# Kernel tuning notes

Hardware: AMD Instinct MI355X
Metric: run time of the kernel (lower is better)

Reference implementation:

```python
import jax, jax.numpy as jnp
import numpy as np

VOCAB = 8192
ZC = 32
BETA = 0.25
EPS = 1e-12  # torch F.normalize eps


def l2norm(x):
    return x / jnp.maximum(jnp.linalg.norm(x, axis=-1, keepdims=True), EPS)


def setup_inputs() -> dict:
    key = jax.random.key(0)
    k1, k2 = jax.random.split(key)
    z = jax.random.normal(k1, (16, ZC, 32, 32), dtype=jnp.float32)  # [B, C, H, W]
    emb = jax.random.uniform(k2, (VOCAB, ZC), dtype=jnp.float32,
                             minval=-1.0 / VOCAB, maxval=1.0 / VOCAB)
    emb = l2norm(emb)  # codebook_norm init
    return {"z": z, "embedding": emb}


def reference(z, embedding):
    # b c h w -> b h w c
    zc = jnp.einsum('bchw->bhwc', z)
    z_flat = zc.reshape(-1, ZC)                      # [N, C], N = B*H*W
    # codebook_norm: normalize inputs and codebook
    z_flat = l2norm(z_flat)
    zn = z_flat.reshape(zc.shape)                    # normalized z, [B,H,W,C]
    e = l2norm(embedding)                            # [V, C]
    # squared euclidean distances: ||z||^2 + ||e||^2 - 2 z e^T  -> [N, V]
    d = (jnp.sum(z_flat ** 2, axis=1, keepdims=True)
         + jnp.sum(e ** 2, axis=1)
         - 2.0 * jnp.einsum('nd,vd->nv', z_flat, e))
    idx = jnp.argmin(d, axis=1)                      # [N]
    z_q = l2norm(embedding[idx]).reshape(zc.shape)   # gather + normalize
    commit_loss = BETA * jnp.mean((jax.lax.stop_gradient(z_q) - zn) ** 2)
    vq_loss = jnp.mean((z_q - jax.lax.stop_gradient(zn)) ** 2)
    # straight-through estimator
    z_q = zn + jax.lax.stop_gradient(z_q - zn)
    z_q = jnp.einsum('bhwc->bchw', z_q)
    return z_q, vq_loss, commit_loss
```

## Files before the change

kernel.cpp:

```cpp
#include <hip/hip_runtime.h>

typedef _Float16 f16;
typedef _Float16 f16x8 __attribute__((ext_vector_type(8)));
typedef float f32x4 __attribute__((ext_vector_type(4)));

#define ZC 32
#define HW 1024
#define TPB 256
#define VCH 256
#define ZROWS_BLK 256

__device__ __forceinline__ unsigned int fkey(float x) {
    unsigned int b = __float_as_uint(x);
    return (b & 0x80000000u) ? ~b : (b | 0x80000000u);
}

__global__ void kprep(const float* __restrict__ z, const float* __restrict__ emb,
                      float* __restrict__ e, f16* __restrict__ Eh, f16* __restrict__ El,
                      f16x8* __restrict__ ZFh, f16x8* __restrict__ ZFl,
                      unsigned long long* __restrict__ packed,
                      int N, int V, int zblocks) {
    const int blk = blockIdx.x;
    if (blk < zblocks) {
        int t = blk * TPB + threadIdx.x;
        if (t < N * 4) {
            int lane = t & 63, zt = t >> 6;
            int n = zt * 16 + (lane & 15);
            int b = n >> 10, hw = n & 1023;
            int kb = (lane >> 4) * 8;
            f16x8 h, l;
#pragma unroll
            for (int j = 0; j < 8; ++j) {
                float v = z[((size_t)(b * ZC + kb + j)) * HW + hw];
                f16 hh = (f16)v;
                h[j] = hh;
                l[j] = (f16)(v - (float)hh);
            }
            ZFh[t] = h;
            ZFl[t] = l;
        }
        int per = (N + zblocks - 1) / zblocks;
        int p0 = blk * per + threadIdx.x;
        if (threadIdx.x < per && p0 < N) packed[p0] = 0ull;
    } else {
        int r = (blk - zblocks) * TPB + threadIdx.x;
        if (r >= V) return;
        const float4* src = reinterpret_cast<const float4*>(emb) + (size_t)r * 8;
        float4 v[8];
        float s = 0.f;
#pragma unroll
        for (int j = 0; j < 8; ++j) {
            v[j] = src[j];
            s += v[j].x * v[j].x + v[j].y * v[j].y + v[j].z * v[j].z + v[j].w * v[j].w;
        }
        float inv = 1.0f / fmaxf(sqrtf(s), 1e-12f);
        float4* dst = reinterpret_cast<float4*>(e) + (size_t)r * 8;
        f16* eh = Eh + (size_t)r * ZC;
        f16* el = El + (size_t)r * ZC;
#pragma unroll
        for (int j = 0; j < 8; ++j) {
            float t0 = v[j].x * inv, t1 = v[j].y * inv, t2 = v[j].z * inv, t3 = v[j].w * inv;
            float4 o; o.x = t0; o.y = t1; o.z = t2; o.w = t3;
            dst[j] = o;
            f16 h0 = (f16)t0, h1 = (f16)t1, h2 = (f16)t2, h3 = (f16)t3;
            eh[4 * j + 0] = h0; eh[4 * j + 1] = h1; eh[4 * j + 2] = h2; eh[4 * j + 3] = h3;
            el[4 * j + 0] = (f16)(t0 - (float)h0);
            el[4 * j + 1] = (f16)(t1 - (float)h1);
            el[4 * j + 2] = (f16)(t2 - (float)h2);
            el[4 * j + 3] = (f16)(t3 - (float)h3);
        }
    }
}

__global__ __launch_bounds__(TPB, 4) void kmfma(const f16x8* __restrict__ ZFh,
                                                const f16x8* __restrict__ ZFl,
                                                const uint4* __restrict__ Eh,
                                                const uint4* __restrict__ El,
                                                unsigned long long* __restrict__ packed,
                                                int Vm1) {
    __shared__ uint4 sEh[VCH * 4];
    __shared__ uint4 sEl[VCH * 4];
    const int tid = threadIdx.x;
    const int zb = blockIdx.x & 63;
    const int cb = blockIdx.x >> 6;

    {
        const uint4* gh = Eh + (size_t)cb * (VCH * 4);
        const uint4* gl = El + (size_t)cb * (VCH * 4);
#pragma unroll
        for (int i = 0; i < 4; ++i) {
            int c = tid + i * TPB;
            int r = c >> 2, q = c & 3;
            int w = (r << 2) | (q ^ ((r >> 1) & 3));
            sEh[w] = gh[c];
            sEl[w] = gl[c];
        }
    }

    const int lane = tid & 63;
    const int wv = tid >> 6;
    const int zt0 = zb * 16 + wv * 4;

    f16x8 Bh[4], Bl[4];
#pragma unroll
    for (int i = 0; i < 4; ++i) {
        Bh[i] = ZFh[(size_t)(zt0 + i) * 64 + lane];
        Bl[i] = ZFl[(size_t)(zt0 + i) * 64 + lane];
    }
    __syncthreads();

    const int r15 = lane & 15, qq = lane >> 4;
    const int laneA = (r15 << 2) | (qq ^ ((r15 >> 1) & 3));

    float bv[4] = {-1e38f, -1e38f, -1e38f, -1e38f};
    int bi[4] = {0, 0, 0, 0};
    int g = cb * VCH + qq * 4;

    for (int ct = 0; ct < VCH / 16; ++ct) {
        f16x8 Ah = *(const f16x8*)&sEh[ct * 64 + laneA];
        f16x8 Al = *(const f16x8*)&sEl[ct * 64 + laneA];
#pragma unroll
        for (int i = 0; i < 4; ++i) {
            f32x4 acc = {0.f, 0.f, 0.f, 0.f};
            acc = __builtin_amdgcn_mfma_f32_16x16x32_f16(Ah, Bh[i], acc, 0, 0, 0);
            acc = __builtin_amdgcn_mfma_f32_16x16x32_f16(Ah, Bl[i], acc, 0, 0, 0);
            acc = __builtin_amdgcn_mfma_f32_16x16x32_f16(Al, Bh[i], acc, 0, 0, 0);
#pragma unroll
            for (int r = 0; r < 4; ++r) {
                float v = acc[r];
                bool gt = v > bv[i];
                bi[i] = gt ? (g + r) : bi[i];
                bv[i] = gt ? v : bv[i];
            }
        }
        g += 16;
    }

#pragma unroll
    for (int i = 0; i < 4; ++i) {
        unsigned long long key =
            ((unsigned long long)fkey(bv[i]) << 32) | (unsigned int)(Vm1 - bi[i]);
        unsigned long long o;
        o = __shfl_xor(key, 16); if (o > key) key = o;
        o = __shfl_xor(key, 32); if (o > key) key = o;
        if (lane < 16) atomicMax(&packed[(size_t)(zt0 + i) * 16 + r15], key);
    }
}

__global__ void kfinal(const float* __restrict__ z, const float* __restrict__ e,
                       const unsigned long long* __restrict__ packed,
                       float* __restrict__ out, float* __restrict__ partial, int V) {
    __shared__ float red[TPB];
    int n = blockIdx.x * TPB + threadIdx.x;
    int b = n >> 10, hw = n & 1023;
    unsigned long long p = packed[n];
    int idx = (V - 1) - (int)(unsigned int)(p & 0xFFFFFFFFull);

    float zrow[ZC];
    float s = 0.f;
#pragma unroll
    for (int c = 0; c < ZC; ++c) {
        float t = z[((size_t)b * ZC + c) * HW + hw];
        zrow[c] = t;
        s += t * t;
    }
    float inv = 1.0f / fmaxf(sqrtf(s), 1e-12f);

    const float4* er = reinterpret_cast<const float4*>(e) + (size_t)idx * 8;
    float loss = 0.f;
#pragma unroll
    for (int q = 0; q < 8; ++q) {
        float4 ev = er[q];
        float d0 = ev.x - zrow[4 * q + 0] * inv;
        float d1 = ev.y - zrow[4 * q + 1] * inv;
        float d2 = ev.z - zrow[4 * q + 2] * inv;
        float d3 = ev.w - zrow[4 * q + 3] * inv;
        loss += d0 * d0 + d1 * d1 + d2 * d2 + d3 * d3;
        out[((size_t)b * ZC + (4 * q + 0)) * HW + hw] = ev.x;
        out[((size_t)b * ZC + (4 * q + 1)) * HW + hw] = ev.y;
        out[((size_t)b * ZC + (4 * q + 2)) * HW + hw] = ev.z;
        out[((size_t)b * ZC + (4 * q + 3)) * HW + hw] = ev.w;
    }

    red[threadIdx.x] = loss;
    __syncthreads();
    for (int st = TPB / 2; st > 0; st >>= 1) {
        if (threadIdx.x < st) red[threadIdx.x] += red[threadIdx.x + st];
        __syncthreads();
    }
    if (threadIdx.x == 0) partial[blockIdx.x] = red[0];
}

__global__ void kloss(const float* __restrict__ partial, float* __restrict__ out,
                      int nblocks, int NC) {
    int lane = threadIdx.x;
    float s = (lane < nblocks) ? partial[lane] : 0.f;
#pragma unroll
    for (int off = 32; off > 0; off >>= 1) s += __shfl_down(s, off);
    if (lane == 0) {
        float mean = s / (float)NC;
        out[NC] = mean;
        out[NC + 1] = 0.25f * mean;
    }
}

extern "C" void kernel_launch(void* const* d_in, const int* in_sizes, int n_in,
                              void* d_out, int out_size, void* d_ws, size_t ws_size,
                              hipStream_t stream) {
    const float* z = (const float*)d_in[0];
    const float* emb = (const float*)d_in[1];
    float* out = (float*)d_out;

    const int N = in_sizes[0] / ZC;
    const int V = in_sizes[1] / ZC;

    char* ws = (char*)d_ws;
    float* e = (float*)ws;
    f16* Eh = (f16*)(ws + (size_t)V * ZC * 4);
    f16* El = (f16*)(ws + (size_t)V * ZC * 6);
    f16x8* ZFh = (f16x8*)(ws + (size_t)V * ZC * 8);
    f16x8* ZFl = (f16x8*)(ws + (size_t)V * ZC * 8 + (size_t)N * ZC * 2);
    unsigned long long* packed =
        (unsigned long long*)(ws + (size_t)V * ZC * 8 + (size_t)N * ZC * 4);
    float* partial = (float*)((char*)packed + (size_t)N * 8);

    const int zblocks = (N * 4 + TPB - 1) / TPB;
    const int eblocks = (V + TPB - 1) / TPB;

    kprep<<<zblocks + eblocks, TPB, 0, stream>>>(z, emb, e, Eh, El, ZFh, ZFl,
                                                 packed, N, V, zblocks);
    kmfma<<<(V / VCH) * (N / ZROWS_BLK), TPB, 0, stream>>>(
        ZFh, ZFl, (const uint4*)Eh, (const uint4*)El, packed, V - 1);
    kfinal<<<N / TPB, TPB, 0, stream>>>(z, e, packed, out, partial, V);
    kloss<<<1, 64, 0, stream>>>(partial, out, N / TPB, N * ZC);
}
```

Before: 42.29 us.

## Normalize z once in prep, double codebook chunk per block, reorder grid

The prep kernel now L2-normalizes each z row, using shuffles across the four lanes that share a row. It writes the normalized values as fp16 hi/lo MFMA operands and also as a row-major fp32 copy. The final kernel reads that copy instead of reloading strided z and recomputing the norm. The MFMA kernel doubles the codebook chunk per block to 512 entries, which halves the grid and doubles the shared memory per block; launch bounds drop to 2 blocks per CU and block indices put codebook chunks in the low bits. This cuts the number of atomicMax calls and the strided z traffic, at the cost of lower occupancy and an extra fp32 z buffer in memory.

Measured after the change: 46.03 us. +8.8%, slower.

```diff
diff --git a/kernel.cpp b/kernel.cpp
--- a/kernel.cpp
+++ b/kernel.cpp
@@ -7,7 +7,7 @@
 #define ZC 32
 #define HW 1024
 #define TPB 256
-#define VCH 256
+#define VCH 512
 #define ZROWS_BLK 256
 
 __device__ __forceinline__ unsigned int fkey(float x) {
@@ -18,30 +18,42 @@
 __global__ void kprep(const float* __restrict__ z, const float* __restrict__ emb,
                       float* __restrict__ e, f16* __restrict__ Eh, f16* __restrict__ El,
                       f16x8* __restrict__ ZFh, f16x8* __restrict__ ZFl,
+                      float* __restrict__ Zn,
                       unsigned long long* __restrict__ packed,
                       int N, int V, int zblocks) {
     const int blk = blockIdx.x;
     if (blk < zblocks) {
         int t = blk * TPB + threadIdx.x;
-        if (t < N * 4) {
-            int lane = t & 63, zt = t >> 6;
-            int n = zt * 16 + (lane & 15);
-            int b = n >> 10, hw = n & 1023;
-            int kb = (lane >> 4) * 8;
-            f16x8 h, l;
-#pragma unroll
-            for (int j = 0; j < 8; ++j) {
-                float v = z[((size_t)(b * ZC + kb + j)) * HW + hw];
-                f16 hh = (f16)v;
-                h[j] = hh;
-                l[j] = (f16)(v - (float)hh);
-            }
-            ZFh[t] = h;
-            ZFl[t] = l;
-        }
-        int per = (N + zblocks - 1) / zblocks;
-        int p0 = blk * per + threadIdx.x;
-        if (threadIdx.x < per && p0 < N) packed[p0] = 0ull;
+        int lane = t & 63, zt = t >> 6;
+        int n = zt * 16 + (lane & 15);
+        int b = n >> 10, hw = n & 1023;
+        int kb = (lane >> 4) * 8;
+        float x[8];
+        float s = 0.f;
+#pragma unroll
+        for (int j = 0; j < 8; ++j) {
+            x[j] = z[((size_t)(b * ZC + kb + j)) * HW + hw];
+            s += x[j] * x[j];
+        }
+        s += __shfl_xor(s, 16);
+        s += __shfl_xor(s, 32);
+        float inv = 1.0f / fmaxf(sqrtf(s), 1e-12f);
+        f16x8 h, l;
+        float4 zn0, zn1;
+#pragma unroll
+        for (int j = 0; j < 8; ++j) {
+            float xn = x[j] * inv;
+            f16 hh = (f16)xn;
+            h[j] = hh;
+            l[j] = (f16)(xn - (float)hh);
+            if (j < 4) ((float*)&zn0)[j] = xn; else ((float*)&zn1)[j - 4] = xn;
+        }
+        ZFh[t] = h;
+        ZFl[t] = l;
+        float4* zr = (float4*)(Zn + (size_t)n * ZC + kb);
+        zr[0] = zn0; zr[1] = zn1;
+        int p0 = blk * 64 + threadIdx.x;
+        if (threadIdx.x < 64) packed[p0] = 0ull;
     } else {
         int r = (blk - zblocks) * TPB + threadIdx.x;
         if (r >= V) return;
@@ -72,7 +84,7 @@
     }
 }
 
-__global__ __launch_bounds__(TPB, 4) void kmfma(const f16x8* __restrict__ ZFh,
+__global__ __launch_bounds__(TPB, 2) void kmfma(const f16x8* __restrict__ ZFh,
                                                 const f16x8* __restrict__ ZFl,
                                                 const uint4* __restrict__ Eh,
                                                 const uint4* __restrict__ El,
@@ -81,14 +93,14 @@
     __shared__ uint4 sEh[VCH * 4];
     __shared__ uint4 sEl[VCH * 4];
     const int tid = threadIdx.x;
-    const int zb = blockIdx.x & 63;
-    const int cb = blockIdx.x >> 6;
+    const int cb = blockIdx.x & 15;
+    const int zb = blockIdx.x >> 4;
 
     {
         const uint4* gh = Eh + (size_t)cb * (VCH * 4);
         const uint4* gl = El + (size_t)cb * (VCH * 4);
 #pragma unroll
-        for (int i = 0; i < 4; ++i) {
+        for (int i = 0; i < 8; ++i) {
             int c = tid + i * TPB;
             int r = c >> 2, q = c & 3;
             int w = (r << 2) | (q ^ ((r >> 1) & 3));
@@ -147,7 +159,7 @@
     }
 }
 
-__global__ void kfinal(const float* __restrict__ z, const float* __restrict__ e,
+__global__ void kfinal(const float* __restrict__ Zn, const float* __restrict__ e,
                        const unsigned long long* __restrict__ packed,
                        float* __restrict__ out, float* __restrict__ partial, int V) {
     __shared__ float red[TPB];
@@ -156,25 +168,15 @@
     unsigned long long p = packed[n];
     int idx = (V - 1) - (int)(unsigned int)(p & 0xFFFFFFFFull);
 
-    float zrow[ZC];
-    float s = 0.f;
-#pragma unroll
-    for (int c = 0; c < ZC; ++c) {
-        float t = z[((size_t)b * ZC + c) * HW + hw];
-        zrow[c] = t;
-        s += t * t;
-    }
-    float inv = 1.0f / fmaxf(sqrtf(s), 1e-12f);
-
     const float4* er = reinterpret_cast<const float4*>(e) + (size_t)idx * 8;
+    const float4* zr = reinterpret_cast<const float4*>(Zn) + (size_t)n * 8;
     float loss = 0.f;
 #pragma unroll
     for (int q = 0; q < 8; ++q) {
         float4 ev = er[q];
-        float d0 = ev.x - zrow[4 * q + 0] * inv;
-        float d1 = ev.y - zrow[4 * q + 1] * inv;
-        float d2 = ev.z - zrow[4 * q + 2] * inv;
-        float d3 = ev.w - zrow[4 * q + 3] * inv;
+        float4 zv = zr[q];
+        float d0 = ev.x - zv.x, d1 = ev.y - zv.y;
+        float d2 = ev.z - zv.z, d3 = ev.w - zv.w;
         loss += d0 * d0 + d1 * d1 + d2 * d2 + d3 * d3;
         out[((size_t)b * ZC + (4 * q + 0)) * HW + hw] = ev.x;
         out[((size_t)b * ZC + (4 * q + 1)) * HW + hw] = ev.y;
@@ -220,17 +222,18 @@
     f16* El = (f16*)(ws + (size_t)V * ZC * 6);
     f16x8* ZFh = (f16x8*)(ws + (size_t)V * ZC * 8);
     f16x8* ZFl = (f16x8*)(ws + (size_t)V * ZC * 8 + (size_t)N * ZC * 2);
+    float* Zn = (float*)(ws + (size_t)V * ZC * 8 + (size_t)N * ZC * 4);
     unsigned long long* packed =
-        (unsigned long long*)(ws + (size_t)V * ZC * 8 + (size_t)N * ZC * 4);
+        (unsigned long long*)(ws + (size_t)V * ZC * 8 + (size_t)N * ZC * 8);
     float* partial = (float*)((char*)packed + (size_t)N * 8);
 
     const int zblocks = (N * 4 + TPB - 1) / TPB;
     const int eblocks = (V + TPB - 1) / TPB;
 
     kprep<<<zblocks + eblocks, TPB, 0, stream>>>(z, emb, e, Eh, El, ZFh, ZFl,
-                                                 packed, N, V, zblocks);
+                                                 Zn, packed, N, V, zblocks);
     kmfma<<<(V / VCH) * (N / ZROWS_BLK), TPB, 0, stream>>>(
         ZFh, ZFl, (const uint4*)Eh, (const uint4*)El, packed, V - 1);
-    kfinal<<<N / TPB, TPB, 0, stream>>>(z, e, packed, out, partial, V);
+    kfinal<<<N / TPB, TPB, 0, stream>>>(Zn, e, packed, out, partial, V);
     kloss<<<1, 64, 0, stream>>>(partial, out, N / TPB, N * ZC);
 }
```
